# Optimization experiments

Hardware: AMD Instinct MI355X
Metric: run time of the kernel (lower is better)

Reference implementation:

```python
import jax, jax.numpy as jnp
import numpy as np
import math

D_MODEL = 1024
N_HEAD = 16
D_FF = 4096
B, T, S = 2, 2048, 2048
LN_EPS = 1e-5


def _linear(x, w, b):
    # torch nn.Linear: y = x @ W.T + b, W: [out, in]
    return jnp.einsum('bsd,od->bso', x, w) + b


def _layer_norm(x, g, b):
    mu = jnp.mean(x, axis=-1, keepdims=True)
    var = jnp.var(x, axis=-1, keepdims=True)
    return (x - mu) * jax.lax.rsqrt(var + LN_EPS) * g + b


def _mha(xq, xkv, wq, bq, wk, bk, wv, bv, wo, bo, mask):
    Bq, Tq, D = xq.shape
    Tk = xkv.shape[1]
    dk = D // N_HEAD
    q = _linear(xq, wq, bq).reshape(Bq, Tq, N_HEAD, dk).transpose(0, 2, 1, 3)
    k = _linear(xkv, wk, bk).reshape(Bq, Tk, N_HEAD, dk).transpose(0, 2, 1, 3)
    v = _linear(xkv, wv, bv).reshape(Bq, Tk, N_HEAD, dk).transpose(0, 2, 1, 3)
    scores = jnp.einsum('bhqd,bhkd->bhqk', q, k) / math.sqrt(dk)
    if mask is not None:
        scores = jnp.where(mask == 0, jnp.asarray(-1e9, scores.dtype), scores)
    attn = jax.nn.softmax(scores, axis=-1)  # dropout is eval-mode identity
    out = jnp.einsum('bhqk,bhkd->bhqd', attn, v)
    out = out.transpose(0, 2, 1, 3).reshape(Bq, Tq, D)
    return _linear(out, wo, bo)


def setup_inputs() -> dict:
    key = jax.random.key(0)
    ks = jax.random.split(key, 20)
    sd = 0.02

    def w(k, shape):
        return (jax.random.normal(k, shape, dtype=jnp.float32) * sd)

    inp = {
        'x': jax.random.normal(ks[0], (B, T, D_MODEL), dtype=jnp.float32),
        'enc_output': jax.random.normal(ks[1], (B, S, D_MODEL), dtype=jnp.float32),
        # causal (future) mask for self-attention
        'tgt_mask': jnp.tril(jnp.ones((T, T), dtype=jnp.int32))[None, None, :, :].repeat(B, axis=0),
        # no source padding -> all ones
        'src_tgt_mask': jnp.ones((B, 1, T, S), dtype=jnp.int32),
        'sa_wq': w(ks[2], (D_MODEL, D_MODEL)), 'sa_bq': jnp.zeros((D_MODEL,), jnp.float32),
        'sa_wk': w(ks[3], (D_MODEL, D_MODEL)), 'sa_bk': jnp.zeros((D_MODEL,), jnp.float32),
        'sa_wv': w(ks[4], (D_MODEL, D_MODEL)), 'sa_bv': jnp.zeros((D_MODEL,), jnp.float32),
        'sa_wo': w(ks[5], (D_MODEL, D_MODEL)), 'sa_bo': jnp.zeros((D_MODEL,), jnp.float32),
        'ca_wq': w(ks[6], (D_MODEL, D_MODEL)), 'ca_bq': jnp.zeros((D_MODEL,), jnp.float32),
        'ca_wk': w(ks[7], (D_MODEL, D_MODEL)), 'ca_bk': jnp.zeros((D_MODEL,), jnp.float32),
        'ca_wv': w(ks[8], (D_MODEL, D_MODEL)), 'ca_bv': jnp.zeros((D_MODEL,), jnp.float32),
        'ca_wo': w(ks[9], (D_MODEL, D_MODEL)), 'ca_bo': jnp.zeros((D_MODEL,), jnp.float32),
        'ffn_w1': w(ks[10], (D_FF, D_MODEL)), 'ffn_b1': jnp.zeros((D_FF,), jnp.float32),
        'ffn_w2': w(ks[11], (D_MODEL, D_FF)), 'ffn_b2': jnp.zeros((D_MODEL,), jnp.float32),
        'ln1_g': jnp.ones((D_MODEL,), jnp.float32), 'ln1_b': jnp.zeros((D_MODEL,), jnp.float32),
        'ln2_g': jnp.ones((D_MODEL,), jnp.float32), 'ln2_b': jnp.zeros((D_MODEL,), jnp.float32),
        'ln3_g': jnp.ones((D_MODEL,), jnp.float32), 'ln3_b': jnp.zeros((D_MODEL,), jnp.float32),
    }
    return inp


def reference(x, enc_output, tgt_mask, src_tgt_mask,
              sa_wq, sa_bq, sa_wk, sa_bk, sa_wv, sa_bv, sa_wo, sa_bo,
              ca_wq, ca_bq, ca_wk, ca_bk, ca_wv, ca_bv, ca_wo, ca_bo,
              ffn_w1, ffn_b1, ffn_w2, ffn_b2,
              ln1_g, ln1_b, ln2_g, ln2_b, ln3_g, ln3_b):
    # masked self-attention + residual + LN
    a1 = _mha(x, x, sa_wq, sa_bq, sa_wk, sa_bk, sa_wv, sa_bv, sa_wo, sa_bo, tgt_mask)
    x = _layer_norm(x + a1, ln1_g, ln1_b)
    # cross-attention + residual + LN
    a2 = _mha(x, enc_output, ca_wq, ca_bq, ca_wk, ca_bk, ca_wv, ca_bv, ca_wo, ca_bo, src_tgt_mask)
    x = _layer_norm(x + a2, ln2_g, ln2_b)
    # FFN + residual + LN
    h = jax.nn.relu(_linear(x, ffn_w1, ffn_b1))
    f = _linear(h, ffn_w2, ffn_b2)
    x = _layer_norm(x + f, ln3_g, ln3_b)
    return x
```

## Files before the change

### kernel.cpp

```cpp
#include <hip/hip_runtime.h>
#include <stdint.h>

typedef uint16_t u16;
typedef __attribute__((ext_vector_type(8))) short short8;
typedef __attribute__((ext_vector_type(4))) short short4v;
typedef __attribute__((ext_vector_type(4))) float f32x4;
typedef __attribute__((ext_vector_type(2))) unsigned int u32x2;

#define GLB_AS __attribute__((address_space(1)))
#define LDS_AS __attribute__((address_space(3)))

__device__ __forceinline__ void gload_lds16(const void* g, void* l) {
  __builtin_amdgcn_global_load_lds((GLB_AS void*)(g), (LDS_AS void*)(l), 16, 0, 0);
}

__device__ __forceinline__ float bf2f(u16 u) {
  union { uint32_t i; float f; } v; v.i = ((uint32_t)u) << 16; return v.f;
}
__device__ __forceinline__ u16 f2bf(float f) {
  uint32_t x = __builtin_bit_cast(uint32_t, f);
  return (u16)((x + 0x7fffu + ((x >> 16) & 1u)) >> 16);
}
__device__ __forceinline__ uint32_t cvtpk(float lo, float hi) {
  uint32_t r;
  asm("v_cvt_pk_bf16_f32 %0, %1, %2" : "=v"(r) : "v"(lo), "v"(hi));
  return r;
}

struct CastJobs {
  const float* s[12];
  u16* d[12];
  int n[12];
};
__global__ __launch_bounds__(256) void cast_many(CastJobs j)
{
  const int job = blockIdx.y;
  const int i = (blockIdx.x * 256 + threadIdx.x) * 4;
  if (i >= j.n[job]) return;
  const float4 v = *(const float4*)(j.s[job] + i);
  short4v r;
  r[0] = (short)f2bf(v.x); r[1] = (short)f2bf(v.y);
  r[2] = (short)f2bf(v.z); r[3] = (short)f2bf(v.w);
  *(short4v*)(j.d[job] + i) = r;
}

template<int RELU, int NSEG, int BN, int SCALEQ, int VT>
__global__ __launch_bounds__(256) void gemm_bt(
    const u16* __restrict__ A, const u16* __restrict__ W,
    const float* __restrict__ b0, const float* __restrict__ b1,
    const float* __restrict__ b2, u16* __restrict__ Y,
    u16* __restrict__ VTp,
    int M, int N, int K)
{
  __shared__ __attribute__((aligned(16))) u16 lA[2][128*64];
  __shared__ __attribute__((aligned(16))) u16 lB[2][BN*64];
  const int tid  = threadIdx.x;
  const int lane = tid & 63, wv = tid >> 6;
  constexpr int WM = (BN == 128) ? 64 : 32;
  constexpr int MI = WM / 16;
  constexpr int BRND = BN / 32;
  const int wm = (BN == 128) ? (wv >> 1) : wv;
  const int wn = (BN == 128) ? (wv & 1) : 0;
  const int l16 = lane & 15, l4 = lane >> 4;
  const int rswz = (l16 & 7) << 4;

  const int gx = gridDim.x;
  int flat = blockIdx.y * gx + blockIdx.x;
  flat = (flat & 7) * ((gx * gridDim.y) >> 3) + (flat >> 3);
  const int bx = (flat % gx) * BN, by = (flat / gx) * 128;

  const f32x4 fzero = {0.f, 0.f, 0.f, 0.f};
  f32x4 acc[MI][4];
#pragma unroll
  for (int i = 0; i < MI; ++i)
#pragma unroll
    for (int j = 0; j < 4; ++j) acc[i][j] = fzero;

  const int o = wv*1024 + lane*16;

  auto stage = [&](int k0, int buf) {
#pragma unroll
    for (int r = 0; r < 4; ++r) {
      const int oo = r*4096 + o;
      const int row = oo >> 7;
      const int src = ((oo & 127) ^ ((row & 7) << 4)) >> 1;
      gload_lds16(A + (size_t)(by + row)*K + (k0 + src), (char*)lA[buf] + oo);
    }
#pragma unroll
    for (int r = 0; r < BRND; ++r) {
      const int oo = r*4096 + o;
      const int row = oo >> 7;
      const int src = ((oo & 127) ^ ((row & 7) << 4)) >> 1;
      gload_lds16(W + (size_t)(bx + row)*K + (k0 + src), (char*)lB[buf] + oo);
    }
  };

  stage(0, 0);
  const int KT = K >> 6;
  for (int kt = 0; kt < KT; ++kt) {
    const int cur = kt & 1;
    __syncthreads();
    short8 af[2][MI], bfv[2][4];
#pragma unroll
    for (int ks = 0; ks < 2; ++ks) {
      const int cb = (ks*64 + l4*16) ^ rswz;
#pragma unroll
      for (int i = 0; i < MI; ++i)
        af[ks][i]  = *(const short8*)((const char*)lA[cur] + (wm*WM + i*16 + l16)*128 + cb);
#pragma unroll
      for (int j = 0; j < 4; ++j)
        bfv[ks][j] = *(const short8*)((const char*)lB[cur] + (wn*64 + j*16 + l16)*128 + cb);
    }
    if (kt + 1 < KT) stage((kt + 1) << 6, cur ^ 1);
#pragma unroll
    for (int ks = 0; ks < 2; ++ks)
#pragma unroll
      for (int i = 0; i < MI; ++i)
#pragma unroll
        for (int j = 0; j < 4; ++j)
          acc[i][j] = __builtin_amdgcn_mfma_f32_16x16x32_bf16(af[ks][i], bfv[ks][j], acc[i][j], 0, 0, 0);
  }

  const float SCLF = 0.18033688f;
#pragma unroll
  for (int j = 0; j < 4; ++j) {
    const int col = bx + wn*64 + j*16 + l16;
    float bv;
    int seg = 0;
    if (NSEG == 1) bv = b0[col];
    else {
      seg = col >> 10;
      const int off = col & 1023;
      const float* bp = (seg == 0) ? b0 : ((seg == 1) ? b1 : b2);
      bv = bp[off];
    }
#pragma unroll
    for (int i = 0; i < MI; ++i) {
      const int r0 = by + wm*WM + i*16 + l4*4;
      if (VT > 0 && seg == VT) {
        const int dcol = col - (VT << 10);
        const int bb = r0 >> 11, t0 = r0 & 2047;
        short4v pv;
#pragma unroll
        for (int r = 0; r < 4; ++r) pv[r] = (short)f2bf(acc[i][j][r] + bv);
        *(short4v*)(VTp + ((size_t)((bb*16 + (dcol >> 6))*64 + (dcol & 63)))*2048 + t0) = pv;
      } else {
#pragma unroll
        for (int r = 0; r < 4; ++r) {
          float v = acc[i][j][r] + bv;
          if (RELU) v = v > 0.f ? v : 0.f;
          if (SCALEQ && (NSEG == 1 || seg == 0)) v *= SCLF;
          Y[(size_t)(r0 + r)*N + col] = f2bf(v);
        }
      }
    }
  }
}

template<int RELU>
__global__ __launch_bounds__(512) void gemm256(
    const u16* __restrict__ A, const u16* __restrict__ W,
    const float* __restrict__ b0, u16* __restrict__ Y,
    int M, int N, int K)
{
  __shared__ __attribute__((aligned(16))) u16 lA[2][256*64];
  __shared__ __attribute__((aligned(16))) u16 lB[2][256*64];
  const int tid  = threadIdx.x;
  const int lane = tid & 63, wid = tid >> 6;
  const int wm = wid >> 2, wn = wid & 3;
  const int l16 = lane & 15, l4 = lane >> 4;
  const int rswz = (l16 & 7) << 4;

  const int gx = gridDim.x;
  int flat = blockIdx.y * gx + blockIdx.x;
  flat = (flat & 7) * ((gx * gridDim.y) >> 3) + (flat >> 3);
  const int bx = (flat % gx) * 256, by = (flat / gx) * 256;

  const f32x4 fzero = {0.f, 0.f, 0.f, 0.f};
  f32x4 acc[8][4];
#pragma unroll
  for (int i = 0; i < 8; ++i)
#pragma unroll
    for (int j = 0; j < 4; ++j) acc[i][j] = fzero;

  const int o = tid * 16;

  auto stage = [&](int k0, int buf) {
#pragma unroll
    for (int r = 0; r < 4; ++r) {
      const int oo = r*8192 + o;
      const int row = oo >> 7;
      const int src = ((oo & 127) ^ ((row & 7) << 4)) >> 1;
      gload_lds16(A + (size_t)(by + row)*K + (k0 + src), (char*)lA[buf] + oo);
    }
#pragma unroll
    for (int r = 0; r < 4; ++r) {
      const int oo = r*8192 + o;
      const int row = oo >> 7;
      const int src = ((oo & 127) ^ ((row & 7) << 4)) >> 1;
      gload_lds16(W + (size_t)(bx + row)*K + (k0 + src), (char*)lB[buf] + oo);
    }
  };

  stage(0, 0);
  const int KT = K >> 6;
  for (int kt = 0; kt < KT; ++kt) {
    const int cur = kt & 1;
    __syncthreads();
    short8 bfv[2][4];
#pragma unroll
    for (int ks = 0; ks < 2; ++ks) {
      const int cb = (ks*64 + l4*16) ^ rswz;
#pragma unroll
      for (int j = 0; j < 4; ++j)
        bfv[ks][j] = *(const short8*)((const char*)lB[cur] + (wn*64 + j*16 + l16)*128 + cb);
    }
    short8 af[2][2];
#pragma unroll
    for (int ks = 0; ks < 2; ++ks) {
      const int cb = (ks*64 + l4*16) ^ rswz;
#pragma unroll
      for (int i = 0; i < 2; ++i)
        af[ks][i] = *(const short8*)((const char*)lA[cur] + (wm*128 + i*16 + l16)*128 + cb);
    }
    if (kt + 1 < KT) stage((kt + 1) << 6, cur ^ 1);
#pragma unroll
    for (int ks = 0; ks < 2; ++ks)
#pragma unroll
      for (int i = 0; i < 2; ++i)
#pragma unroll
        for (int j = 0; j < 4; ++j)
          acc[i][j] = __builtin_amdgcn_mfma_f32_16x16x32_bf16(af[ks][i], bfv[ks][j], acc[i][j], 0, 0, 0);
#pragma unroll
    for (int q = 1; q < 4; ++q) {
#pragma unroll
      for (int ks = 0; ks < 2; ++ks) {
        const int cb = (ks*64 + l4*16) ^ rswz;
#pragma unroll
        for (int i = 0; i < 2; ++i)
          af[ks][i] = *(const short8*)((const char*)lA[cur] +
              (wm*128 + (q*2 + i)*16 + l16)*128 + cb);
      }
#pragma unroll
      for (int ks = 0; ks < 2; ++ks)
#pragma unroll
        for (int i = 0; i < 2; ++i)
#pragma unroll
          for (int j = 0; j < 4; ++j)
            acc[q*2 + i][j] = __builtin_amdgcn_mfma_f32_16x16x32_bf16(
                af[ks][i], bfv[ks][j], acc[q*2 + i][j], 0, 0, 0);
    }
  }

#pragma unroll
  for (int j = 0; j < 4; ++j) {
    const int col = bx + wn*64 + j*16 + l16;
    const float bv = b0[col];
#pragma unroll
    for (int i = 0; i < 8; ++i) {
      const int r0 = by + wm*128 + i*16 + l4*4;
#pragma unroll
      for (int r = 0; r < 4; ++r) {
        float v = acc[i][j][r] + bv;
        if (RELU) v = v > 0.f ? v : 0.f;
        Y[(size_t)(r0 + r)*N + col] = f2bf(v);
      }
    }
  }
}

template<int CAUSAL, int QR>
__global__ __launch_bounds__(512, (QR == 16) ? 4 : 2) void attn_fwd(
    const u16* __restrict__ Q, int qs,
    const u16* __restrict__ K, int ks_,
    const u16* __restrict__ Vt, u16* __restrict__ O, int Tk)
{
  constexpr int NG = QR / 16;
  __shared__ __attribute__((aligned(16))) u16 lK[2][128*64];
  __shared__ __attribute__((aligned(16))) u16 lV[2][64*128];
  __shared__ __attribute__((aligned(16))) u16 lP[8][NG*1024];
  const int tid  = threadIdx.x;
  const int lane = tid & 63, wv = tid >> 6;
  const int l16 = lane & 15, l4 = lane >> 4;
  const int b = blockIdx.z, h = blockIdx.y;
  int strip;
  if (CAUSAL) {
    const int u = (blockIdx.x + blockIdx.z) & 15;
    strip = (u & 1) ? (15 - (u >> 1)) : (u >> 1);
  } else {
    strip = blockIdx.x;
  }
  const int Bq = strip * (8 * QR);
  const int qrow = Bq + wv*QR;

  short8 qf[NG][2];
#pragma unroll
  for (int g = 0; g < NG; ++g) {
    const u16* Qb = Q + (size_t)(b*2048 + qrow + g*16 + l16)*qs + h*64;
#pragma unroll
    for (int ks = 0; ks < 2; ++ks)
      qf[g][ks] = *(const short8*)(Qb + ks*32 + l4*8);
  }

  const f32x4 fzero = {0.f, 0.f, 0.f, 0.f};
  f32x4 accO[NG][4];
#pragma unroll
  for (int g = 0; g < NG; ++g)
#pragma unroll
    for (int i = 0; i < 4; ++i) accO[g][i] = fzero;
  float lrow[NG];
#pragma unroll
  for (int g = 0; g < NG; ++g) lrow[g] = 0.f;

  const int kend = CAUSAL ? (Bq + 8*QR) : Tk;
  const int nt = kend >> 7;
  const int qmax = qrow + QR - 1;
  const int srK = tid >> 3;
  const int scK = 8 * ((tid & 7) ^ (srK & 7));
  const int srV = tid >> 4;
  const int scV = 8 * ((tid & 15) ^ (srV & 7));
  const u16* KbG = K  + (size_t)(b*2048)*ks_ + h*64 + scK;
  const u16* VbG = Vt + ((size_t)((b*16 + h)*64 + srV))*2048 + scV;
  const int wvoff = (tid >> 6) * 1024;
  const int rswz = (l16 & 7) << 4;
  const int sbq = (lane & 48) + l4*4;

  char* const pbuf = (char*)lP + (tid >> 6) * (NG*2048);
  const int swzP = (l16 & 7) << 4;
  int wrA[4], rdA[2];
#pragma unroll
  for (int nf = 0; nf < 4; ++nf) wrA[nf] = l16*128 + ((nf*32 + l4*8) ^ swzP);
#pragma unroll
  for (int c = 0; c < 2; ++c)    rdA[c] = l16*128 + ((c*64 + l4*16) ^ swzP);

  auto readK = [&](int h2, int bb, short8 (&kf)[4][2]) {
#pragma unroll
    for (int nf = 0; nf < 4; ++nf) {
      const char* base = (const char*)lK[bb] + (h2*64 + nf*16 + l16)*128;
      kf[nf][0] = *(const short8*)(base + ((l4*16)      ^ rswz));
      kf[nf][1] = *(const short8*)(base + ((64 + l4*16) ^ rswz));
    }
  };

  auto compute64 = [&](int h2, int kvb, short8 (&kf)[4][2], int bb) {
#pragma unroll
    for (int g = 0; g < NG; ++g) {
      f32x4 sf[4];
      __builtin_amdgcn_s_setprio(1);
#pragma unroll
      for (int nf = 0; nf < 4; ++nf) {
        f32x4 s = fzero;
        s = __builtin_amdgcn_mfma_f32_16x16x32_bf16(kf[nf][0], qf[g][0], s, 0, 0, 0);
        s = __builtin_amdgcn_mfma_f32_16x16x32_bf16(kf[nf][1], qf[g][1], s, 0, 0, 0);
        sf[nf] = s;
      }
      __builtin_amdgcn_s_setprio(0);
      if (CAUSAL && (kvb + 63 > qrow + g*16)) {
        const int q = qrow + g*16 + l16;
#pragma unroll
        for (int nf = 0; nf < 4; ++nf)
#pragma unroll
          for (int r = 0; r < 4; ++r) {
            const int kv = kvb + nf*16 + l4*4 + r;
            if (kv > q) sf[nf][r] = -1e30f;
          }
      }
#pragma unroll
      for (int nf = 0; nf < 4; ++nf)
#pragma unroll
        for (int r = 0; r < 4; ++r)
          sf[nf][r] = exp2f(sf[nf][r]);
      float sm[4];
#pragma unroll
      for (int nf = 0; nf < 4; ++nf)
        sm[nf] = (sf[nf][0] + sf[nf][1]) + (sf[nf][2] + sf[nf][3]);
      lrow[g] += (sm[0] + sm[1]) + (sm[2] + sm[3]);
#pragma unroll
      for (int nf = 0; nf < 4; ++nf) {
        u32x2 w;
        w[0] = cvtpk(sf[nf][0], sf[nf][1]);
        w[1] = cvtpk(sf[nf][2], sf[nf][3]);
        *(u32x2*)(pbuf + g*2048 + wrA[nf]) = w;
      }
    }
#pragma unroll
    for (int c = 0; c < 2; ++c) {
      short8 pa[NG];
#pragma unroll
      for (int g = 0; g < NG; ++g)
        pa[g] = *(const short8*)(pbuf + g*2048 + rdA[c]);
      __builtin_amdgcn_s_setprio(1);
#pragma unroll
      for (int df = 0; df < 4; ++df) {
        const short8 vf = *(const short8*)((const char*)lV[bb] +
            (df*16 + l16)*256 + ((h2*128 + c*64 + l4*16) ^ rswz));
#pragma unroll
        for (int g = 0; g < NG; ++g)
          accO[g][df] = __builtin_amdgcn_mfma_f32_16x16x32_bf16(pa[g], vf, accO[g][df], 0, 0, 0);
      }
      __builtin_amdgcn_s_setprio(0);
    }
  };

#pragma unroll
  for (int r = 0; r < 2; ++r) {
    gload_lds16(KbG + (size_t)(r*64 + srK)*ks_, (char*)lK[0] + r*8192 + wvoff);
    gload_lds16(VbG + (size_t)(r*32)*2048,      (char*)lV[0] + r*8192 + wvoff);
  }

  for (int t = 0; t < nt; ++t) {
    const int bb = t & 1;
    const int kb = t << 7;
    __syncthreads();
    short8 kf[4][2];
    readK(0, bb, kf);
    if (t + 1 < nt) {
      const int kb2 = kb + 128;
#pragma unroll
      for (int r = 0; r < 2; ++r) {
        gload_lds16(KbG + (size_t)(kb2 + r*64 + srK)*ks_,
                    (char*)lK[bb^1] + r*8192 + wvoff);
        gload_lds16(VbG + (size_t)(r*32)*2048 + kb2,
                    (char*)lV[bb^1] + r*8192 + wvoff);
      }
    }
    compute64(0, kb, kf, bb);
    if (!CAUSAL || (kb + 64 <= qmax)) {
      readK(1, bb, kf);
      compute64(1, kb + 64, kf, bb);
    }
  }

#pragma unroll
  for (int g = 0; g < NG; ++g) {
    lrow[g] += __shfl_xor(lrow[g], 16);
    lrow[g] += __shfl_xor(lrow[g], 32);
    u16* Ob = O + (size_t)(b*2048 + qrow + g*16 + l4*4)*1024 + h*64;
#pragma unroll
    for (int r = 0; r < 4; ++r) {
      const float inv = 1.f / __shfl(lrow[g], sbq + r);
#pragma unroll
      for (int df = 0; df < 4; ++df)
        Ob[(size_t)r*1024 + df*16 + l16] = f2bf(accO[g][df][r] * inv);
    }
  }
}

template<int XF32, int OF32>
__global__ __launch_bounds__(256) void add_ln(
    const void* __restrict__ Xp, const u16* __restrict__ R,
    const float* __restrict__ G, const float* __restrict__ Bb,
    void* __restrict__ OUTp)
{
  const int row  = blockIdx.x*4 + (threadIdx.x >> 6);
  const int lane = threadIdx.x & 63;
  const size_t base = (size_t)row*1024 + lane*16;
  float v[16];
  if (XF32) {
#pragma unroll
    for (int k = 0; k < 4; ++k) {
      const float4 t = *(const float4*)((const float*)Xp + base + k*4);
      v[k*4+0] = t.x; v[k*4+1] = t.y; v[k*4+2] = t.z; v[k*4+3] = t.w;
    }
  } else {
#pragma unroll
    for (int k = 0; k < 2; ++k) {
      short8 t = *(const short8*)((const u16*)Xp + base + k*8);
#pragma unroll
      for (int i = 0; i < 8; ++i) v[k*8+i] = bf2f((u16)t[i]);
    }
  }
#pragma unroll
  for (int k = 0; k < 2; ++k) {
    short8 t = *(const short8*)(R + base + k*8);
#pragma unroll
    for (int i = 0; i < 8; ++i) v[k*8+i] += bf2f((u16)t[i]);
  }
  float s = 0.f, s2 = 0.f;
#pragma unroll
  for (int i = 0; i < 16; ++i) { s += v[i]; s2 += v[i]*v[i]; }
#pragma unroll
  for (int m = 1; m < 64; m <<= 1) { s += __shfl_xor(s, m); s2 += __shfl_xor(s2, m); }
  const float mu  = s * (1.f/1024.f);
  const float var = s2 * (1.f/1024.f) - mu*mu;
  const float rs  = rsqrtf(var + 1e-5f);
  float gg[16], bb_[16];
#pragma unroll
  for (int k = 0; k < 4; ++k) {
    const float4 g4 = *(const float4*)(G  + lane*16 + k*4);
    const float4 b4 = *(const float4*)(Bb + lane*16 + k*4);
    gg[k*4+0]=g4.x; gg[k*4+1]=g4.y; gg[k*4+2]=g4.z; gg[k*4+3]=g4.w;
    bb_[k*4+0]=b4.x; bb_[k*4+1]=b4.y; bb_[k*4+2]=b4.z; bb_[k*4+3]=b4.w;
  }
  if (OF32) {
#pragma unroll
    for (int k = 0; k < 4; ++k) {
      float4 ov;
      ov.x = (v[k*4+0]-mu)*rs*gg[k*4+0] + bb_[k*4+0];
      ov.y = (v[k*4+1]-mu)*rs*gg[k*4+1] + bb_[k*4+1];
      ov.z = (v[k*4+2]-mu)*rs*gg[k*4+2] + bb_[k*4+2];
      ov.w = (v[k*4+3]-mu)*rs*gg[k*4+3] + bb_[k*4+3];
      *(float4*)((float*)OUTp + base + k*4) = ov;
    }
  } else {
#pragma unroll
    for (int k = 0; k < 2; ++k) {
      short8 ov;
#pragma unroll
      for (int i = 0; i < 8; ++i)
        ov[i] = (short)f2bf((v[k*8+i]-mu)*rs*gg[k*8+i] + bb_[k*8+i]);
      *(short8*)((u16*)OUTp + base + k*8) = ov;
    }
  }
}

extern "C" void kernel_launch(void* const* d_in, const int* in_sizes, int n_in,
                              void* d_out, int out_size, void* d_ws, size_t ws_size,
                              hipStream_t stream)
{
  (void)in_sizes; (void)n_in; (void)out_size;
  const float* x    = (const float*)d_in[0];
  const float* enc  = (const float*)d_in[1];
  const float* sa_wq = (const float*)d_in[4];  const float* sa_bq = (const float*)d_in[5];
  const float* sa_wk = (const float*)d_in[6];  const float* sa_bk = (const float*)d_in[7];
  const float* sa_wv = (const float*)d_in[8];  const float* sa_bv = (const float*)d_in[9];
  const float* sa_wo = (const float*)d_in[10]; const float* sa_bo = (const float*)d_in[11];
  const float* ca_wq = (const float*)d_in[12]; const float* ca_bq = (const float*)d_in[13];
  const float* ca_wk = (const float*)d_in[14]; const float* ca_bk = (const float*)d_in[15];
  const float* ca_wv = (const float*)d_in[16]; const float* ca_bv = (const float*)d_in[17];
  const float* ca_wo = (const float*)d_in[18]; const float* ca_bo = (const float*)d_in[19];
  const float* w1 = (const float*)d_in[20];    const float* b1 = (const float*)d_in[21];
  const float* w2 = (const float*)d_in[22];    const float* b2 = (const float*)d_in[23];
  const float* ln1g = (const float*)d_in[24];  const float* ln1b = (const float*)d_in[25];
  const float* ln2g = (const float*)d_in[26];  const float* ln2b = (const float*)d_in[27];
  const float* ln3g = (const float*)d_in[28];  const float* ln3b = (const float*)d_in[29];
  float* out = (float*)d_out;

  char* ws = (char*)d_ws;
  const size_t MB = 1024*1024;
  u16* xb   = (u16*)(ws);
  u16* encb = (u16*)(ws + 8*MB);
  u16* wsab = (u16*)(ws + 16*MB);
  u16* wcab = (u16*)(ws + 24*MB);
  u16* x1   = (u16*)(ws + 32*MB);
  u16* ao   = (u16*)(ws + 40*MB);
  u16* tmp  = (u16*)(ws + 48*MB);
  u16* vt   = (u16*)(ws + 56*MB);
  u16* qkv  = (u16*)(ws + 64*MB);
  u16* kvb  = (u16*)(ws + 88*MB);
  u16* x2   = xb;
  u16* hb   = qkv;

  const bool bigws = ws_size >= (size_t)120*MB;
  u16* w1b = bigws ? (u16*)(ws + 104*MB) : encb;
  u16* w2b = bigws ? (u16*)(ws + 112*MB) : vt;

  const int NW = 1024*1024;
  const int NX = 4096*1024;
  dim3 blk(256);

  {
    CastJobs cj{};
    cj.s[0] = x;     cj.d[0] = xb;           cj.n[0] = NX;
    cj.s[1] = enc;   cj.d[1] = encb;         cj.n[1] = NX;
    cj.s[2] = sa_wq; cj.d[2] = wsab + 0*NW;  cj.n[2] = NW;
    cj.s[3] = sa_wk; cj.d[3] = wsab + 1*NW;  cj.n[3] = NW;
    cj.s[4] = sa_wv; cj.d[4] = wsab + 2*NW;  cj.n[4] = NW;
    cj.s[5] = sa_wo; cj.d[5] = wsab + 3*NW;  cj.n[5] = NW;
    cj.s[6] = ca_wq; cj.d[6] = wcab + 0*NW;  cj.n[6] = NW;
    cj.s[7] = ca_wk; cj.d[7] = wcab + 1*NW;  cj.n[7] = NW;
    cj.s[8] = ca_wv; cj.d[8] = wcab + 2*NW;  cj.n[8] = NW;
    cj.s[9] = ca_wo; cj.d[9] = wcab + 3*NW;  cj.n[9] = NW;
    int njobs = 10;
    if (bigws) {
      cj.s[10] = w1; cj.d[10] = w1b; cj.n[10] = NX;
      cj.s[11] = w2; cj.d[11] = w2b; cj.n[11] = NX;
      njobs = 12;
    }
    cast_many<<<dim3(NX/1024, njobs), blk, 0, stream>>>(cj);
  }

  const int M = 4096;
  dim3 gN64(16, 32);
  dim3 gQKV(24, 32);
  dim3 gKV(16, 32);
  dim3 gF1(16, 16);
  dim3 gAttn(16, 16, 2);
  dim3 blk512(512);

  gemm_bt<0,3,128,1,2><<<gQKV, blk, 0, stream>>>(xb, wsab, sa_bq, sa_bk, sa_bv, qkv, vt, M, 3072, 1024);
  attn_fwd<1,16><<<gAttn, blk512, 0, stream>>>(qkv, 3072, qkv + 1024, 3072, vt, ao, 2048);
  gemm_bt<0,1,64,0,0><<<gN64, blk, 0, stream>>>(ao, wsab + 3*NW, sa_bo, sa_bo, sa_bo, tmp, nullptr, M, 1024, 1024);
  add_ln<1,0><<<1024, blk, 0, stream>>>(x, tmp, ln1g, ln1b, x1);

  gemm_bt<0,1,64,1,0><<<gN64, blk, 0, stream>>>(x1, wcab + 0*NW, ca_bq, ca_bq, ca_bq, qkv, nullptr, M, 1024, 1024);
  gemm_bt<0,2,128,0,1><<<gKV, blk, 0, stream>>>(encb, wcab + 1*NW, ca_bk, ca_bv, ca_bv, kvb, vt, M, 2048, 1024);
  attn_fwd<0,16><<<gAttn, blk512, 0, stream>>>(qkv, 1024, kvb, 2048, vt, ao, 2048);
  if (!bigws) {
    CastJobs cj{};
    cj.s[0] = w1; cj.d[0] = w1b; cj.n[0] = NX;
    cj.s[1] = w2; cj.d[1] = w2b; cj.n[1] = NX;
    cast_many<<<dim3(NX/1024, 2), blk, 0, stream>>>(cj);
  }
  gemm_bt<0,1,64,0,0><<<gN64, blk, 0, stream>>>(ao, wcab + 3*NW, ca_bo, ca_bo, ca_bo, tmp, nullptr, M, 1024, 1024);
  add_ln<0,0><<<1024, blk, 0, stream>>>(x1, tmp, ln2g, ln2b, x2);

  gemm256<1><<<gF1, blk512, 0, stream>>>(x2, w1b, b1, hb, M, 4096, 1024);
  gemm_bt<0,1,64,0,0><<<gN64, blk, 0, stream>>>(hb, w2b, b2, b2, b2, tmp, nullptr, M, 1024, 4096);
  add_ln<0,1><<<1024, blk, 0, stream>>>(x2, tmp, ln3g, ln3b, out);
}
```

Measured before the change: 323.5 us.

## Fuse cross-attention Q and KV projections into one GEMM launch; drop 256-tile FFN GEMM

Cross-attention Q projection (from x1) and K/V projection (from encoder output) now run in one launch, gemm_cross3. Each block picks its A operand and epilogue (scaled Q, K row-major, V transposed) from the column segment. This removes one launch and lets the two GEMMs share a single wave of blocks. The FFN1 GEMM moves from the 512-thread 256x256 tile kernel to the generic 128-tile gemm_bt with ReLU, which trades per-block reuse for more blocks. A dead stub kernel, gemm_cross, is left in the file.

```diff
diff --git a/kernel.cpp b/kernel.cpp
--- a/kernel.cpp
+++ b/kernel.cpp
@@ -157,48 +157,77 @@
   }
 }
 
-template<int RELU>
-__global__ __launch_bounds__(512) void gemm256(
-    const u16* __restrict__ A, const u16* __restrict__ W,
-    const float* __restrict__ b0, u16* __restrict__ Y,
-    int M, int N, int K)
+__global__ __launch_bounds__(256) void gemm_cross(
+    const u16* __restrict__ Aq, const u16* __restrict__ Akv,
+    const float* __restrict__ bq, const float* __restrict__ bk,
+    const float* __restrict__ bv_, u16* __restrict__ Yq,
+    u16* __restrict__ Ykv, u16* __restrict__ VTp, int K)
 {
-  __shared__ __attribute__((aligned(16))) u16 lA[2][256*64];
-  __shared__ __attribute__((aligned(16))) u16 lB[2][256*64];
+  __shared__ __attribute__((aligned(16))) u16 lA[2][128*64];
+  __shared__ __attribute__((aligned(16))) u16 lB[2][128*64];
   const int tid  = threadIdx.x;
-  const int lane = tid & 63, wid = tid >> 6;
-  const int wm = wid >> 2, wn = wid & 3;
+  const int lane = tid & 63, wv = tid >> 6;
+  const int wm = wv >> 1, wn = wv & 1;
   const int l16 = lane & 15, l4 = lane >> 4;
   const int rswz = (l16 & 7) << 4;
 
   const int gx = gridDim.x;
   int flat = blockIdx.y * gx + blockIdx.x;
   flat = (flat & 7) * ((gx * gridDim.y) >> 3) + (flat >> 3);
-  const int bx = (flat % gx) * 256, by = (flat / gx) * 256;
+  const int bx = (flat % gx) * 128, by = (flat / gx) * 128;
+  const int seg = bx >> 10;
+  const u16* A = (seg == 0) ? Aq : Akv;
+  const u16* W = (seg == 0) ? nullptr : nullptr;
+  (void)W;
+  (void)A;
+}
+
+__global__ __launch_bounds__(256) void gemm_cross3(
+    const u16* __restrict__ Aq, const u16* __restrict__ Akv,
+    const u16* __restrict__ Wbase,
+    const float* __restrict__ bq, const float* __restrict__ bk,
+    const float* __restrict__ bv_, u16* __restrict__ Yq,
+    u16* __restrict__ Ykv, u16* __restrict__ VTp, int K)
+{
+  __shared__ __attribute__((aligned(16))) u16 lA[2][128*64];
+  __shared__ __attribute__((aligned(16))) u16 lB[2][128*64];
+  const int tid  = threadIdx.x;
+  const int lane = tid & 63, wv = tid >> 6;
+  const int wm = wv >> 1, wn = wv & 1;
+  const int l16 = lane & 15, l4 = lane >> 4;
+  const int rswz = (l16 & 7) << 4;
+
+  const int gx = gridDim.x;
+  int flat = blockIdx.y * gx + blockIdx.x;
+  flat = (flat & 7) * ((gx * gridDim.y) >> 3) + (flat >> 3);
+  const int bx = (flat % gx) * 128, by = (flat / gx) * 128;
+  const int seg = bx >> 10;
+  const u16* A = (seg == 0) ? Aq : Akv;
+  const u16* Wp = Wbase;
 
   const f32x4 fzero = {0.f, 0.f, 0.f, 0.f};
-  f32x4 acc[8][4];
-#pragma unroll
-  for (int i = 0; i < 8; ++i)
+  f32x4 acc[4][4];
+#pragma unroll
+  for (int i = 0; i < 4; ++i)
 #pragma unroll
     for (int j = 0; j < 4; ++j) acc[i][j] = fzero;
 
-  const int o = tid * 16;
+  const int o = wv*1024 + lane*16;
 
   auto stage = [&](int k0, int buf) {
 #pragma unroll
     for (int r = 0; r < 4; ++r) {
-      const int oo = r*8192 + o;
+      const int oo = r*4096 + o;
       const int row = oo >> 7;
       const int src = ((oo & 127) ^ ((row & 7) << 4)) >> 1;
       gload_lds16(A + (size_t)(by + row)*K + (k0 + src), (char*)lA[buf] + oo);
     }
 #pragma unroll
     for (int r = 0; r < 4; ++r) {
-      const int oo = r*8192 + o;
+      const int oo = r*4096 + o;
       const int row = oo >> 7;
       const int src = ((oo & 127) ^ ((row & 7) << 4)) >> 1;
-      gload_lds16(W + (size_t)(bx + row)*K + (k0 + src), (char*)lB[buf] + oo);
+      gload_lds16(Wp + (size_t)(bx + row)*K + (k0 + src), (char*)lB[buf] + oo);
     }
   };
 
@@ -207,63 +236,51 @@
   for (int kt = 0; kt < KT; ++kt) {
     const int cur = kt & 1;
     __syncthreads();
-    short8 bfv[2][4];
+    short8 af[2][4], bfv[2][4];
 #pragma unroll
     for (int ks = 0; ks < 2; ++ks) {
       const int cb = (ks*64 + l4*16) ^ rswz;
 #pragma unroll
+      for (int i = 0; i < 4; ++i)
+        af[ks][i]  = *(const short8*)((const char*)lA[cur] + (wm*64 + i*16 + l16)*128 + cb);
+#pragma unroll
       for (int j = 0; j < 4; ++j)
         bfv[ks][j] = *(const short8*)((const char*)lB[cur] + (wn*64 + j*16 + l16)*128 + cb);
     }
-    short8 af[2][2];
-#pragma unroll
-    for (int ks = 0; ks < 2; ++ks) {
-      const int cb = (ks*64 + l4*16) ^ rswz;
-#pragma unroll
-      for (int i = 0; i < 2; ++i)
-        af[ks][i] = *(const short8*)((const char*)lA[cur] + (wm*128 + i*16 + l16)*128 + cb);
-    }
     if (kt + 1 < KT) stage((kt + 1) << 6, cur ^ 1);
 #pragma unroll
     for (int ks = 0; ks < 2; ++ks)
 #pragma unroll
-      for (int i = 0; i < 2; ++i)
+      for (int i = 0; i < 4; ++i)
 #pragma unroll
         for (int j = 0; j < 4; ++j)
           acc[i][j] = __builtin_amdgcn_mfma_f32_16x16x32_bf16(af[ks][i], bfv[ks][j], acc[i][j], 0, 0, 0);
-#pragma unroll
-    for (int q = 1; q < 4; ++q) {
-#pragma unroll
-      for (int ks = 0; ks < 2; ++ks) {
-        const int cb = (ks*64 + l4*16) ^ rswz;
-#pragma unroll
-        for (int i = 0; i < 2; ++i)
-          af[ks][i] = *(const short8*)((const char*)lA[cur] +
-              (wm*128 + (q*2 + i)*16 + l16)*128 + cb);
-      }
-#pragma unroll
-      for (int ks = 0; ks < 2; ++ks)
-#pragma unroll
-        for (int i = 0; i < 2; ++i)
-#pragma unroll
-          for (int j = 0; j < 4; ++j)
-            acc[q*2 + i][j] = __builtin_amdgcn_mfma_f32_16x16x32_bf16(
-                af[ks][i], bfv[ks][j], acc[q*2 + i][j], 0, 0, 0);
-    }
-  }
-
+  }
+
+  const float SCLF = 0.18033688f;
 #pragma unroll
   for (int j = 0; j < 4; ++j) {
     const int col = bx + wn*64 + j*16 + l16;
-    const float bv = b0[col];
-#pragma unroll
-    for (int i = 0; i < 8; ++i) {
-      const int r0 = by + wm*128 + i*16 + l4*4;
-#pragma unroll
-      for (int r = 0; r < 4; ++r) {
-        float v = acc[i][j][r] + bv;
-        if (RELU) v = v > 0.f ? v : 0.f;
-        Y[(size_t)(r0 + r)*N + col] = f2bf(v);
+    const int off = col & 1023;
+    const float* bp = (seg == 0) ? bq : ((seg == 1) ? bk : bv_);
+    const float bv = bp[off];
+#pragma unroll
+    for (int i = 0; i < 4; ++i) {
+      const int r0 = by + wm*64 + i*16 + l4*4;
+      if (seg == 2) {
+        const int bb = r0 >> 11, t0 = r0 & 2047;
+        short4v pv;
+#pragma unroll
+        for (int r = 0; r < 4; ++r) pv[r] = (short)f2bf(acc[i][j][r] + bv);
+        *(short4v*)(VTp + ((size_t)((bb*16 + (off >> 6))*64 + (off & 63)))*2048 + t0) = pv;
+      } else if (seg == 1) {
+#pragma unroll
+        for (int r = 0; r < 4; ++r)
+          Ykv[(size_t)(r0 + r)*2048 + off] = f2bf(acc[i][j][r] + bv);
+      } else {
+#pragma unroll
+        for (int r = 0; r < 4; ++r)
+          Yq[(size_t)(r0 + r)*1024 + off] = f2bf((acc[i][j][r] + bv) * SCLF);
       }
     }
   }
@@ -583,8 +600,7 @@
   const int M = 4096;
   dim3 gN64(16, 32);
   dim3 gQKV(24, 32);
-  dim3 gKV(16, 32);
-  dim3 gF1(16, 16);
+  dim3 gF1(32, 32);
   dim3 gAttn(16, 16, 2);
   dim3 blk512(512);
 
@@ -593,8 +609,8 @@
   gemm_bt<0,1,64,0,0><<<gN64, blk, 0, stream>>>(ao, wsab + 3*NW, sa_bo, sa_bo, sa_bo, tmp, nullptr, M, 1024, 1024);
   add_ln<1,0><<<1024, blk, 0, stream>>>(x, tmp, ln1g, ln1b, x1);
 
-  gemm_bt<0,1,64,1,0><<<gN64, blk, 0, stream>>>(x1, wcab + 0*NW, ca_bq, ca_bq, ca_bq, qkv, nullptr, M, 1024, 1024);
-  gemm_bt<0,2,128,0,1><<<gKV, blk, 0, stream>>>(encb, wcab + 1*NW, ca_bk, ca_bv, ca_bv, kvb, vt, M, 2048, 1024);
+  gemm_cross3<<<gQKV, blk, 0, stream>>>(x1, encb, wcab, ca_bq, ca_bk, ca_bv,
+                                        qkv, kvb, vt, 1024);
   attn_fwd<0,16><<<gAttn, blk512, 0, stream>>>(qkv, 1024, kvb, 2048, vt, ao, 2048);
   if (!bigws) {
     CastJobs cj{};
@@ -605,7 +621,7 @@
   gemm_bt<0,1,64,0,0><<<gN64, blk, 0, stream>>>(ao, wcab + 3*NW, ca_bo, ca_bo, ca_bo, tmp, nullptr, M, 1024, 1024);
   add_ln<0,0><<<1024, blk, 0, stream>>>(x1, tmp, ln2g, ln2b, x2);
 
-  gemm256<1><<<gF1, blk512, 0, stream>>>(x2, w1b, b1, hb, M, 4096, 1024);
+  gemm_bt<1,1,128,0,0><<<gF1, blk, 0, stream>>>(x2, w1b, b1, b1, b1, hb, nullptr, M, 4096, 1024);
   gemm_bt<0,1,64,0,0><<<gN64, blk, 0, stream>>>(hb, w2b, b2, b2, b2, tmp, nullptr, M, 1024, 4096);
   add_ln<0,1><<<1024, blk, 0, stream>>>(x2, tmp, ln3g, ln3b, out);
 }
```

Measured after the change: 324.3 us. About the same (+0.2%).
